# Kernel tuning notes

Measured on AMD Instinct MI355X. Metric: run time of the kernel, lower is better.

The kernel has to match this reference:

```python
import jax, jax.numpy as jnp
import numpy as np

BATCH, IN_DIM, GRID, OUT_DIM = 2048, 512, 32, 512


def setup_inputs() -> dict:
    key = jax.random.key(0)
    k_x, k_c = jax.random.split(key)
    x = jax.random.normal(k_x, (BATCH, IN_DIM), dtype=jnp.float32)
    fourier_coeffs = jax.random.normal(k_c, (2, IN_DIM, GRID, OUT_DIM), dtype=jnp.float32) / np.sqrt(GRID * OUT_DIM)
    bias = jnp.zeros((1, OUT_DIM), dtype=jnp.float32)
    return {"x": x, "fourier_coeffs": fourier_coeffs, "bias": bias}


def reference(x, fourier_coeffs, bias):
    # freqs: 1..GRID, shape (GRID,)
    freqs = jnp.arange(1, GRID + 1, dtype=x.dtype)
    kx = x[..., None] * freqs            # [B, I, G]
    cos_t = jnp.cos(kx)
    sin_t = jnp.sin(kx)
    # Equivalent to broadcast-multiply with coeffs then sum over grid and input dims:
    y = (jnp.einsum('big,igo->bo', cos_t, fourier_coeffs[0])
         + jnp.einsum('big,igo->bo', sin_t, fourier_coeffs[1]))
    return y + bias
```

## Files before the change

kernel.cpp:

```cpp
#include <hip/hip_runtime.h>
#include <hip/hip_bf16.h>
#include <stdint.h>

namespace {

constexpr int IDIM   = 512;
constexpr int ODIM   = 512;
constexpr int KTOT   = 32768;
constexpr int BM = 128, BN = 128, BK = 64;
constexpr int SPLITK = 8;
constexpr int KCHUNK = KTOT / SPLITK;
constexpr int NSTEP  = KCHUNK / BK;

typedef short    bf16x8 __attribute__((ext_vector_type(8)));
typedef float    f32x4  __attribute__((ext_vector_type(4)));
typedef float    f32x2  __attribute__((ext_vector_type(2)));
typedef uint32_t u32x4  __attribute__((ext_vector_type(4)));

__device__ __forceinline__ uint32_t f2bf1(float f) {
  union { float f; uint32_t u; } v; v.f = f;
  return (v.u + 0x7fffu + ((v.u >> 16) & 1u)) >> 16;
}
__device__ __forceinline__ uint32_t pk2(float lo, float hi) {
  return f2bf1(lo) | (f2bf1(hi) << 16);
}

__device__ __forceinline__ uint32_t pk2f(float lo, float hi) {
  union { float f; uint32_t u; } a, b; a.f = lo; b.f = hi;
  return __builtin_amdgcn_perm(b.u + 0x8000u, a.u + 0x8000u, 0x07060302u);
}

__device__ __forceinline__ void gload_lds16(const void* gsrc, const char* ldsdst) {
  __builtin_amdgcn_global_load_lds(
      (const __attribute__((address_space(1))) uint32_t*)(uintptr_t)gsrc,
      (__attribute__((address_space(3))) uint32_t*)(uint32_t)(uintptr_t)ldsdst,
      16, 0, 0);
}

#define WAIT_LGKM0   asm volatile("s_waitcnt lgkmcnt(0)" ::: "memory")
#define WAIT_VM(N)   asm volatile("s_waitcnt vmcnt(" #N ")" ::: "memory")
#define FENCE        asm volatile("" ::: "memory")

__global__ __launch_bounds__(256) void transpose_convert_kernel(const float* __restrict__ fc,
                                                                uint16_t* __restrict__ wt) {
  const int t = threadIdx.x, lane = t & 63, wave = t >> 6;
  const int bid = blockIdx.x;
  const int ot = bid & 3;
  const int kt = bid >> 2;
  const int o0 = ot * 128 + lane * 2;
  const int kb = kt * 128 + wave * 32;
  const float* src = fc + (size_t)kb * ODIM + o0;
  uint32_t w0[16], w1[16];
#pragma unroll
  for (int p = 0; p < 16; ++p) {
    f32x2 a = *(const f32x2*)(src + (size_t)(2 * p) * ODIM);
    f32x2 b = *(const f32x2*)(src + (size_t)(2 * p + 1) * ODIM);
    w0[p] = pk2(a.x, b.x);
    w1[p] = pk2(a.y, b.y);
  }
  uint16_t* dst0 = wt + (size_t)o0 * KTOT + kb;
  uint16_t* dst1 = dst0 + KTOT;
#pragma unroll
  for (int c = 0; c < 4; ++c) {
    *(u32x4*)(dst0 + c * 8) = *(const u32x4*)&w0[c * 4];
    *(u32x4*)(dst1 + c * 8) = *(const u32x4*)&w1[c * 4];
  }
}

__global__ __launch_bounds__(256) void init_bias_kernel(const float* __restrict__ bias,
                                                        float* __restrict__ out) {
  int i = blockIdx.x * 256 + threadIdx.x;
  ((f32x4*)out)[i] = ((const f32x4*)bias)[i & 127];
}

__global__ __launch_bounds__(256, 2) void fkan_gemm_kernel(const float* __restrict__ x,
                                                           const uint16_t* __restrict__ wt,
                                                           float* __restrict__ out) {
  __shared__ char lds[81920];

  const int t    = threadIdx.x;
  const int lane = t & 63;
  const int wave = t >> 6;

  int bid = blockIdx.x;
  int swz = (bid & 7) * 64 + (bid >> 3);
  const int bm = swz & 15;
  const int bn = (swz >> 4) & 3;
  const int bz = swz >> 6;

  const int row0  = bm * BM;
  const int col0  = bn * BN;
  const int kc0   = bz * KCHUNK;
  const int sflag = bz >> 2;
  const int ibase = (bz & 3) * 128;

  const int gr   = t & 127;
  const int ioff = t >> 7;
  const float* xp = x + (size_t)(row0 + gr) * IDIM + ibase + ioff;
  int awoff[4];
#pragma unroll
  for (int j = 0; j < 4; ++j)
    awoff[j] = gr * 128 + (((ioff * 4 + j) ^ (gr & 7)) << 4);

  const uint16_t* wptr[4];
  int wdst[4];
#pragma unroll
  for (int q = 0; q < 4; ++q) {
    int nl   = q * 32 + wave * 8 + (lane >> 3);
    int slot = lane & 7;
    wptr[q] = wt + (size_t)(col0 + nl) * KTOT + kc0 + ((slot ^ (nl & 7)) << 3);
    wdst[q] = q * 4096 + wave * 1024;
  }

  const int wm = wave >> 1, wn = wave & 1;
  int arow[4], ar7[4], bcol[4], bc7[4];
#pragma unroll
  for (int m = 0; m < 4; ++m) {
    int rr = wm * 64 + m * 16 + (lane & 15);
    arow[m] = rr * 128; ar7[m] = rr & 7;
    int cc = wn * 64 + m * 16 + (lane & 15);
    bcol[m] = cc * 128; bc7[m] = cc & 7;
  }

  f32x4 acc[4][4] = {};

  auto stageW = [&](int buf) {
#pragma unroll
    for (int q = 0; q < 4; ++q) {
      gload_lds16(wptr[q], lds + 32768 + buf * 16384 + wdst[q]);
      wptr[q] += BK;
    }
  };

  auto genA = [&](int abuf, float ang) {
    float s1, c1;
    __sincosf(ang, &s1, &c1);
    const float c2 = 2.f * c1 * c1 - 1.f;
    const float s2 = 2.f * s1 * c1;
    const float k2 = 2.f * c2;
    float po  = sflag ? s1   : c1;
    float pe  = sflag ? s2   : c2;
    float pom = sflag ? -s1  : c1;
    float pem = sflag ? 0.f  : 1.f;
    char* ab = lds + abuf * 16384;
#pragma unroll
    for (int grp = 0; grp < 4; ++grp) {
      u32x4 w;
#pragma unroll
      for (int u = 0; u < 4; ++u) {
        w[u] = pk2f(po, pe);
        float no = k2 * po - pom; pom = po; po = no;
        float ne = k2 * pe - pem; pem = pe; pe = ne;
      }
      *(u32x4*)(ab + awoff[grp]) = w;
    }
  };

  auto compute = [&](int wbuf, int abuf) {
    const char* ab = lds + abuf * 16384;
    const char* wb = lds + 32768 + wbuf * 16384;
#pragma unroll
    for (int ks = 0; ks < 2; ++ks) {
      const int ksb = ks * 4 + (lane >> 4);
      bf16x8 af[4], bfr[4];
#pragma unroll
      for (int m = 0; m < 4; ++m)
        af[m] = *(const bf16x8*)(ab + arow[m] + ((ksb ^ ar7[m]) << 4));
#pragma unroll
      for (int n = 0; n < 4; ++n)
        bfr[n] = *(const bf16x8*)(wb + bcol[n] + ((ksb ^ bc7[n]) << 4));
#pragma unroll
      for (int m = 0; m < 4; ++m)
#pragma unroll
        for (int n = 0; n < 4; ++n)
          acc[m][n] = __builtin_amdgcn_mfma_f32_16x16x32_bf16(af[m], bfr[n], acc[m][n], 0, 0, 0);
    }
  };

  float angCur  = xp[0];
  float angNext = xp[2];
  stageW(0);
  stageW(1);
  genA(0, angCur);
  WAIT_VM(4);
  WAIT_LGKM0;
  __builtin_amdgcn_s_barrier();
  FENCE;

  int wb_c = 0;
  int ws_c = 2;
  for (int st = 0; st < NSTEP; ++st) {
    const int ab = st & 1;
    if (st + 2 < NSTEP) {
      stageW(ws_c);
      ws_c = (ws_c == 2) ? 0 : ws_c + 1;
    }
    if (st + 1 < NSTEP) {
      float a = angNext;
      if (st + 2 < NSTEP) angNext = xp[2 * (st + 2)];
      genA(ab ^ 1, a);
    }
    compute(wb_c, ab);
    wb_c = (wb_c == 2) ? 0 : wb_c + 1;
    if (st + 1 < NSTEP) {
      WAIT_LGKM0;
      if (st + 2 < NSTEP) { WAIT_VM(4); } else { WAIT_VM(0); }
      __builtin_amdgcn_s_barrier();
      FENCE;
    }
  }

#pragma unroll
  for (int m = 0; m < 4; ++m) {
#pragma unroll
    for (int n = 0; n < 4; ++n) {
      int rr = row0 + wm * 64 + m * 16 + ((lane >> 4) << 2);
      int cc = col0 + wn * 64 + n * 16 + (lane & 15);
#pragma unroll
      for (int j = 0; j < 4; ++j)
        atomicAdd(out + (size_t)(rr + j) * ODIM + cc, acc[m][n][j]);
    }
  }
}

}

extern "C" void kernel_launch(void* const* d_in, const int* in_sizes, int n_in,
                              void* d_out, int out_size, void* d_ws, size_t ws_size,
                              hipStream_t stream) {
  const float* x    = (const float*)d_in[0];
  const float* fc   = (const float*)d_in[1];
  const float* bias = (const float*)d_in[2];
  float*    out = (float*)d_out;
  uint16_t* wt  = (uint16_t*)d_ws;

  transpose_convert_kernel<<<1024, 256, 0, stream>>>(fc, wt);
  init_bias_kernel<<<1024, 256, 0, stream>>>(bias, out);
  fkan_gemm_kernel<<<512, 256, 0, stream>>>(x, wt, out);
}
```

Before: 198.7 us.

## Fuse fp32-to-bf16 weight transpose into GEMM via register-staged loads

Removes the separate transpose/convert pre-pass that wrote a bf16 transposed copy of the coefficients to workspace. The GEMM now reads fp32 coefficients directly with per-lane strided loads into registers, converts them to bf16, and writes them to LDS in the swizzled layout. The weight pipeline goes from a triple-buffered async global-to-LDS scheme to double buffering through registers. This saves one full pass over the 64MB coefficient tensor, but the GEMM now reads twice the bytes per weight, holds 32 extra registers per thread, and exposes load latency behind a full vmcnt(0) wait each step.

```diff
diff --git a/kernel.cpp b/kernel.cpp
--- a/kernel.cpp
+++ b/kernel.cpp
@@ -14,58 +14,16 @@
 
 typedef short    bf16x8 __attribute__((ext_vector_type(8)));
 typedef float    f32x4  __attribute__((ext_vector_type(4)));
-typedef float    f32x2  __attribute__((ext_vector_type(2)));
 typedef uint32_t u32x4  __attribute__((ext_vector_type(4)));
-
-__device__ __forceinline__ uint32_t f2bf1(float f) {
-  union { float f; uint32_t u; } v; v.f = f;
-  return (v.u + 0x7fffu + ((v.u >> 16) & 1u)) >> 16;
-}
-__device__ __forceinline__ uint32_t pk2(float lo, float hi) {
-  return f2bf1(lo) | (f2bf1(hi) << 16);
-}
 
 __device__ __forceinline__ uint32_t pk2f(float lo, float hi) {
   union { float f; uint32_t u; } a, b; a.f = lo; b.f = hi;
   return __builtin_amdgcn_perm(b.u + 0x8000u, a.u + 0x8000u, 0x07060302u);
 }
 
-__device__ __forceinline__ void gload_lds16(const void* gsrc, const char* ldsdst) {
-  __builtin_amdgcn_global_load_lds(
-      (const __attribute__((address_space(1))) uint32_t*)(uintptr_t)gsrc,
-      (__attribute__((address_space(3))) uint32_t*)(uint32_t)(uintptr_t)ldsdst,
-      16, 0, 0);
-}
-
 #define WAIT_LGKM0   asm volatile("s_waitcnt lgkmcnt(0)" ::: "memory")
-#define WAIT_VM(N)   asm volatile("s_waitcnt vmcnt(" #N ")" ::: "memory")
+#define WAIT_VM0     asm volatile("s_waitcnt vmcnt(0)" ::: "memory")
 #define FENCE        asm volatile("" ::: "memory")
-
-__global__ __launch_bounds__(256) void transpose_convert_kernel(const float* __restrict__ fc,
-                                                                uint16_t* __restrict__ wt) {
-  const int t = threadIdx.x, lane = t & 63, wave = t >> 6;
-  const int bid = blockIdx.x;
-  const int ot = bid & 3;
-  const int kt = bid >> 2;
-  const int o0 = ot * 128 + lane * 2;
-  const int kb = kt * 128 + wave * 32;
-  const float* src = fc + (size_t)kb * ODIM + o0;
-  uint32_t w0[16], w1[16];
-#pragma unroll
-  for (int p = 0; p < 16; ++p) {
-    f32x2 a = *(const f32x2*)(src + (size_t)(2 * p) * ODIM);
-    f32x2 b = *(const f32x2*)(src + (size_t)(2 * p + 1) * ODIM);
-    w0[p] = pk2(a.x, b.x);
-    w1[p] = pk2(a.y, b.y);
-  }
-  uint16_t* dst0 = wt + (size_t)o0 * KTOT + kb;
-  uint16_t* dst1 = dst0 + KTOT;
-#pragma unroll
-  for (int c = 0; c < 4; ++c) {
-    *(u32x4*)(dst0 + c * 8) = *(const u32x4*)&w0[c * 4];
-    *(u32x4*)(dst1 + c * 8) = *(const u32x4*)&w1[c * 4];
-  }
-}
 
 __global__ __launch_bounds__(256) void init_bias_kernel(const float* __restrict__ bias,
                                                         float* __restrict__ out) {
@@ -74,9 +32,9 @@
 }
 
 __global__ __launch_bounds__(256, 2) void fkan_gemm_kernel(const float* __restrict__ x,
-                                                           const uint16_t* __restrict__ wt,
+                                                           const float* __restrict__ fc,
                                                            float* __restrict__ out) {
-  __shared__ char lds[81920];
+  __shared__ char lds[65536];
 
   const int t    = threadIdx.x;
   const int lane = t & 63;
@@ -102,14 +60,15 @@
   for (int j = 0; j < 4; ++j)
     awoff[j] = gr * 128 + (((ioff * 4 + j) ^ (gr & 7)) << 4);
 
-  const uint16_t* wptr[4];
-  int wdst[4];
+  int wko[4], wo[4], wldso[4];
 #pragma unroll
   for (int q = 0; q < 4; ++q) {
-    int nl   = q * 32 + wave * 8 + (lane >> 3);
-    int slot = lane & 7;
-    wptr[q] = wt + (size_t)(col0 + nl) * KTOT + kc0 + ((slot ^ (nl & 7)) << 3);
-    wdst[q] = q * 4096 + wave * 1024;
+    int idx = wave * 4 + q;
+    wko[q] = idx >> 1;
+    wo[q]  = (idx & 1) * 64 + lane;
+    int o = wo[q];
+    wldso[q] = (o >> 5) * 4096 + ((o >> 3) & 3) * 1024 +
+               (((o & 7) * 8 + (wko[q] ^ (o & 7))) << 4);
   }
 
   const int wm = wave >> 1, wn = wave & 1;
@@ -123,12 +82,27 @@
   }
 
   f32x4 acc[4][4] = {};
-
-  auto stageW = [&](int buf) {
+  float r[4][8];
+
+  auto stageLoad = [&](int st) {
+    const float* base = fc + (size_t)(kc0 + st * BK) * ODIM + col0;
 #pragma unroll
     for (int q = 0; q < 4; ++q) {
-      gload_lds16(wptr[q], lds + 32768 + buf * 16384 + wdst[q]);
-      wptr[q] += BK;
+      const float* s = base + (size_t)(wko[q] * 8) * ODIM + wo[q];
+#pragma unroll
+      for (int j = 0; j < 8; ++j)
+        r[q][j] = s[(size_t)j * ODIM];
+    }
+  };
+
+  auto stageWrite = [&](int buf) {
+#pragma unroll
+    for (int q = 0; q < 4; ++q) {
+      u32x4 w;
+#pragma unroll
+      for (int u = 0; u < 4; ++u)
+        w[u] = pk2f(r[q][2 * u], r[q][2 * u + 1]);
+      *(u32x4*)(lds + 32768 + buf * 16384 + wldso[q]) = w;
     }
   };
 
@@ -156,9 +130,9 @@
     }
   };
 
-  auto compute = [&](int wbuf, int abuf) {
-    const char* ab = lds + abuf * 16384;
-    const char* wb = lds + 32768 + wbuf * 16384;
+  auto compute = [&](int par) {
+    const char* ab = lds + par * 16384;
+    const char* wb = lds + 32768 + par * 16384;
 #pragma unroll
     for (int ks = 0; ks < 2; ++ks) {
       const int ksb = ks * 4 + (lane >> 4);
@@ -179,35 +153,32 @@
 
   float angCur  = xp[0];
   float angNext = xp[2];
-  stageW(0);
-  stageW(1);
+  stageLoad(0);
   genA(0, angCur);
-  WAIT_VM(4);
+  WAIT_VM0;
+  stageWrite(0);
   WAIT_LGKM0;
   __builtin_amdgcn_s_barrier();
   FENCE;
 
-  int wb_c = 0;
-  int ws_c = 2;
+  int par = 0;
   for (int st = 0; st < NSTEP; ++st) {
-    const int ab = st & 1;
-    if (st + 2 < NSTEP) {
-      stageW(ws_c);
-      ws_c = (ws_c == 2) ? 0 : ws_c + 1;
-    }
     if (st + 1 < NSTEP) {
+      stageLoad(st + 1);
       float a = angNext;
-      if (st + 2 < NSTEP) angNext = xp[2 * (st + 2)];
-      genA(ab ^ 1, a);
-    }
-    compute(wb_c, ab);
-    wb_c = (wb_c == 2) ? 0 : wb_c + 1;
+      int pf = (st + 2 < NSTEP) ? (st + 2) : (NSTEP - 1);
+      angNext = xp[2 * pf];
+      genA(par ^ 1, a);
+    }
+    compute(par);
     if (st + 1 < NSTEP) {
+      WAIT_VM0;
+      stageWrite(par ^ 1);
       WAIT_LGKM0;
-      if (st + 2 < NSTEP) { WAIT_VM(4); } else { WAIT_VM(0); }
       __builtin_amdgcn_s_barrier();
       FENCE;
     }
+    par ^= 1;
   }
 
 #pragma unroll
@@ -232,9 +203,8 @@
   const float* fc   = (const float*)d_in[1];
   const float* bias = (const float*)d_in[2];
   float*    out = (float*)d_out;
-  uint16_t* wt  = (uint16_t*)d_ws;
-
-  transpose_convert_kernel<<<1024, 256, 0, stream>>>(fc, wt);
+  (void)d_ws; (void)ws_size;
+
   init_bias_kernel<<<1024, 256, 0, stream>>>(bias, out);
-  fkan_gemm_kernel<<<512, 256, 0, stream>>>(x, wt, out);
-}
+  fkan_gemm_kernel<<<512, 256, 0, stream>>>(x, fc, out);
+}
```

Result: slower. 212.0 us (+6.7%).

## Generate Fourier A fragments in registers instead of staging through LDS

Applied to the files above, without the earlier changes.

Each wave now builds its own bf16 cos/sin MFMA A-fragments in registers. It loads x values directly and uses a sincos plus Chebyshev recurrence per fragment, instead of writing a shared A tile to LDS and reading it back. This removes the A-tile LDS stores and reads and shrinks shared memory from 80KB to 48KB. The main loop becomes a two-step unrolled loop with double-buffered x registers and a single vmcnt wait. The cost is extra VALU work: more sincos calls, and the trig generation is duplicated across the two waves that share rows. The vmcnt(8) wait also forces the newest weight stage to finish earlier than strictly needed.

```diff
diff --git a/kernel.cpp b/kernel.cpp
--- a/kernel.cpp
+++ b/kernel.cpp
@@ -24,7 +24,6 @@
 __device__ __forceinline__ uint32_t pk2(float lo, float hi) {
   return f2bf1(lo) | (f2bf1(hi) << 16);
 }
-
 __device__ __forceinline__ uint32_t pk2f(float lo, float hi) {
   union { float f; uint32_t u; } a, b; a.f = lo; b.f = hi;
   return __builtin_amdgcn_perm(b.u + 0x8000u, a.u + 0x8000u, 0x07060302u);
@@ -37,7 +36,6 @@
       16, 0, 0);
 }
 
-#define WAIT_LGKM0   asm volatile("s_waitcnt lgkmcnt(0)" ::: "memory")
 #define WAIT_VM(N)   asm volatile("s_waitcnt vmcnt(" #N ")" ::: "memory")
 #define FENCE        asm volatile("" ::: "memory")
 
@@ -76,11 +74,13 @@
 __global__ __launch_bounds__(256, 2) void fkan_gemm_kernel(const float* __restrict__ x,
                                                            const uint16_t* __restrict__ wt,
                                                            float* __restrict__ out) {
-  __shared__ char lds[81920];
+  __shared__ char lds[49152];
 
   const int t    = threadIdx.x;
   const int lane = t & 63;
   const int wave = t >> 6;
+  const int lid  = lane & 15;
+  const int hb   = lane >> 4;
 
   int bid = blockIdx.x;
   int swz = (bid & 7) * 64 + (bid >> 3);
@@ -94,14 +94,6 @@
   const int sflag = bz >> 2;
   const int ibase = (bz & 3) * 128;
 
-  const int gr   = t & 127;
-  const int ioff = t >> 7;
-  const float* xp = x + (size_t)(row0 + gr) * IDIM + ibase + ioff;
-  int awoff[4];
-#pragma unroll
-  for (int j = 0; j < 4; ++j)
-    awoff[j] = gr * 128 + (((ioff * 4 + j) ^ (gr & 7)) << 4);
-
   const uint16_t* wptr[4];
   int wdst[4];
 #pragma unroll
@@ -113,59 +105,69 @@
   }
 
   const int wm = wave >> 1, wn = wave & 1;
-  int arow[4], ar7[4], bcol[4], bc7[4];
-#pragma unroll
-  for (int m = 0; m < 4; ++m) {
-    int rr = wm * 64 + m * 16 + (lane & 15);
-    arow[m] = rr * 128; ar7[m] = rr & 7;
-    int cc = wn * 64 + m * 16 + (lane & 15);
-    bcol[m] = cc * 128; bc7[m] = cc & 7;
-  }
-
-  f32x4 acc[4][4] = {};
+  int bcol[4], bc7[4];
+#pragma unroll
+  for (int n = 0; n < 4; ++n) {
+    int cc = wn * 64 + n * 16 + lid;
+    bcol[n] = cc * 128; bc7[n] = cc & 7;
+  }
+
+  const float* xb0 = x + (size_t)(row0 + wm * 64 + lid) * IDIM + ibase;
+  const float n0f = (float)(hb * 8 + 1);
+
+  f32x4  acc[4][4] = {};
+  bf16x8 af[2][4];
 
   auto stageW = [&](int buf) {
 #pragma unroll
     for (int q = 0; q < 4; ++q) {
-      gload_lds16(wptr[q], lds + 32768 + buf * 16384 + wdst[q]);
+      gload_lds16(wptr[q], lds + buf * 16384 + wdst[q]);
       wptr[q] += BK;
     }
   };
 
-  auto genA = [&](int abuf, float ang) {
-    float s1, c1;
-    __sincosf(ang, &s1, &c1);
-    const float c2 = 2.f * c1 * c1 - 1.f;
-    const float s2 = 2.f * s1 * c1;
-    const float k2 = 2.f * c2;
-    float po  = sflag ? s1   : c1;
-    float pe  = sflag ? s2   : c2;
-    float pom = sflag ? -s1  : c1;
-    float pem = sflag ? 0.f  : 1.f;
-    char* ab = lds + abuf * 16384;
-#pragma unroll
-    for (int grp = 0; grp < 4; ++grp) {
-      u32x4 w;
-#pragma unroll
-      for (int u = 0; u < 4; ++u) {
-        w[u] = pk2f(po, pe);
-        float no = k2 * po - pom; pom = po; po = no;
-        float ne = k2 * pe - pem; pem = pe; pe = ne;
+  auto loadX = [&](float (&dst)[4][2], int st) {
+#pragma unroll
+    for (int m = 0; m < 4; ++m) {
+      const float* p = xb0 + (size_t)(m * 16) * IDIM + st * 2;
+      dst[m][0] = p[0]; dst[m][1] = p[1];
+    }
+  };
+
+  auto genAll = [&](const float (&xc)[4][2]) {
+#pragma unroll
+    for (int m = 0; m < 4; ++m) {
+#pragma unroll
+      for (int ks = 0; ks < 2; ++ks) {
+        float xx = xc[m][ks];
+        float s1, c1; __sincosf(xx, &s1, &c1);
+        float sn, cn; __sincosf(n0f * xx, &sn, &cn);
+        const float k2 = 2.f * c1;
+        float cur, prev;
+        if (sflag == 0) { cur = cn; prev = fmaf(cn, c1,  sn * s1); }
+        else            { cur = sn; prev = fmaf(sn, c1, -cn * s1); }
+        float v[8];
+        v[0] = cur;
+#pragma unroll
+        for (int j = 1; j < 8; ++j) {
+          float nx = fmaf(k2, cur, -prev);
+          prev = cur; cur = nx; v[j] = nx;
+        }
+        union { u32x4 u4; bf16x8 b8; } cvt;
+#pragma unroll
+        for (int u = 0; u < 4; ++u)
+          cvt.u4[u] = pk2f(v[2 * u], v[2 * u + 1]);
+        af[ks][m] = cvt.b8;
       }
-      *(u32x4*)(ab + awoff[grp]) = w;
-    }
-  };
-
-  auto compute = [&](int wbuf, int abuf) {
-    const char* ab = lds + abuf * 16384;
-    const char* wb = lds + 32768 + wbuf * 16384;
+    }
+  };
+
+  auto compute = [&](int wbuf) {
+    const char* wb = lds + wbuf * 16384;
 #pragma unroll
     for (int ks = 0; ks < 2; ++ks) {
-      const int ksb = ks * 4 + (lane >> 4);
-      bf16x8 af[4], bfr[4];
-#pragma unroll
-      for (int m = 0; m < 4; ++m)
-        af[m] = *(const bf16x8*)(ab + arow[m] + ((ksb ^ ar7[m]) << 4));
+      const int ksb = ks * 4 + hb;
+      bf16x8 bfr[4];
 #pragma unroll
       for (int n = 0; n < 4; ++n)
         bfr[n] = *(const bf16x8*)(wb + bcol[n] + ((ksb ^ bc7[n]) << 4));
@@ -173,41 +175,35 @@
       for (int m = 0; m < 4; ++m)
 #pragma unroll
         for (int n = 0; n < 4; ++n)
-          acc[m][n] = __builtin_amdgcn_mfma_f32_16x16x32_bf16(af[m], bfr[n], acc[m][n], 0, 0, 0);
-    }
-  };
-
-  float angCur  = xp[0];
-  float angNext = xp[2];
+          acc[m][n] = __builtin_amdgcn_mfma_f32_16x16x32_bf16(af[ks][m], bfr[n], acc[m][n], 0, 0, 0);
+    }
+  };
+
+  float xA[4][2], xB[4][2];
+
+  loadX(xA, 0);
   stageW(0);
   stageW(1);
-  genA(0, angCur);
   WAIT_VM(4);
-  WAIT_LGKM0;
   __builtin_amdgcn_s_barrier();
   FENCE;
 
-  int wb_c = 0;
-  int ws_c = 2;
-  for (int st = 0; st < NSTEP; ++st) {
-    const int ab = st & 1;
-    if (st + 2 < NSTEP) {
-      stageW(ws_c);
-      ws_c = (ws_c == 2) ? 0 : ws_c + 1;
-    }
+  auto iter = [&](int st, const float (&xcur)[4][2], float (&xnxt)[4][2]) {
+    if (st + 2 < NSTEP) stageW((st + 2) % 3);
+    if (st + 1 < NSTEP) loadX(xnxt, st + 1);
+    genAll(xcur);
+    compute(st % 3);
     if (st + 1 < NSTEP) {
-      float a = angNext;
-      if (st + 2 < NSTEP) angNext = xp[2 * (st + 2)];
-      genA(ab ^ 1, a);
-    }
-    compute(wb_c, ab);
-    wb_c = (wb_c == 2) ? 0 : wb_c + 1;
-    if (st + 1 < NSTEP) {
-      WAIT_LGKM0;
-      if (st + 2 < NSTEP) { WAIT_VM(4); } else { WAIT_VM(0); }
+      WAIT_VM(8);
       __builtin_amdgcn_s_barrier();
       FENCE;
     }
+  };
+
+#pragma unroll 1
+  for (int st2 = 0; st2 < NSTEP; st2 += 2) {
+    iter(st2,     xA, xB);
+    iter(st2 + 1, xB, xA);
   }
 
 #pragma unroll
@@ -215,7 +211,7 @@
 #pragma unroll
     for (int n = 0; n < 4; ++n) {
       int rr = row0 + wm * 64 + m * 16 + ((lane >> 4) << 2);
-      int cc = col0 + wn * 64 + n * 16 + (lane & 15);
+      int cc = col0 + wn * 64 + n * 16 + lid;
 #pragma unroll
       for (int j = 0; j < 4; ++j)
         atomicAdd(out + (size_t)(rr + j) * ODIM + cc, acc[m][n][j]);
```

After: 248.2 us. 1.25x slower.

## Load B fragments directly from global into registers, drop LDS staging

Applied to the files above, without the earlier changes.

Weight tiles are no longer staged through LDS with global_load_lds and a triple buffer. Each wave now loads its MFMA B fragments straight from global memory into double-buffered registers, one step ahead. This shrinks LDS from 80KB to 32KB and removes the LDS reads for B, but each weight element is now loaded twice, once per wave row (wm). It also adds register pressure and waits on vmcnt(0) every step, which reduces how much loads overlap with compute.

```diff
diff --git a/kernel.cpp b/kernel.cpp
--- a/kernel.cpp
+++ b/kernel.cpp
@@ -24,21 +24,13 @@
 __device__ __forceinline__ uint32_t pk2(float lo, float hi) {
   return f2bf1(lo) | (f2bf1(hi) << 16);
 }
-
 __device__ __forceinline__ uint32_t pk2f(float lo, float hi) {
   union { float f; uint32_t u; } a, b; a.f = lo; b.f = hi;
   return __builtin_amdgcn_perm(b.u + 0x8000u, a.u + 0x8000u, 0x07060302u);
 }
 
-__device__ __forceinline__ void gload_lds16(const void* gsrc, const char* ldsdst) {
-  __builtin_amdgcn_global_load_lds(
-      (const __attribute__((address_space(1))) uint32_t*)(uintptr_t)gsrc,
-      (__attribute__((address_space(3))) uint32_t*)(uint32_t)(uintptr_t)ldsdst,
-      16, 0, 0);
-}
-
 #define WAIT_LGKM0   asm volatile("s_waitcnt lgkmcnt(0)" ::: "memory")
-#define WAIT_VM(N)   asm volatile("s_waitcnt vmcnt(" #N ")" ::: "memory")
+#define WAIT_VM0     asm volatile("s_waitcnt vmcnt(0)" ::: "memory")
 #define FENCE        asm volatile("" ::: "memory")
 
 __global__ __launch_bounds__(256) void transpose_convert_kernel(const float* __restrict__ fc,
@@ -76,11 +68,13 @@
 __global__ __launch_bounds__(256, 2) void fkan_gemm_kernel(const float* __restrict__ x,
                                                            const uint16_t* __restrict__ wt,
                                                            float* __restrict__ out) {
-  __shared__ char lds[81920];
+  __shared__ char lds[32768];
 
   const int t    = threadIdx.x;
   const int lane = t & 63;
   const int wave = t >> 6;
+  const int lid  = lane & 15;
+  const int hb   = lane >> 4;
 
   int bid = blockIdx.x;
   int swz = (bid & 7) * 64 + (bid >> 3);
@@ -102,34 +96,27 @@
   for (int j = 0; j < 4; ++j)
     awoff[j] = gr * 128 + (((ioff * 4 + j) ^ (gr & 7)) << 4);
 
-  const uint16_t* wptr[4];
-  int wdst[4];
-#pragma unroll
-  for (int q = 0; q < 4; ++q) {
-    int nl   = q * 32 + wave * 8 + (lane >> 3);
-    int slot = lane & 7;
-    wptr[q] = wt + (size_t)(col0 + nl) * KTOT + kc0 + ((slot ^ (nl & 7)) << 3);
-    wdst[q] = q * 4096 + wave * 1024;
-  }
-
   const int wm = wave >> 1, wn = wave & 1;
-  int arow[4], ar7[4], bcol[4], bc7[4];
+  int arow[4], ar7[4];
 #pragma unroll
   for (int m = 0; m < 4; ++m) {
-    int rr = wm * 64 + m * 16 + (lane & 15);
+    int rr = wm * 64 + m * 16 + lid;
     arow[m] = rr * 128; ar7[m] = rr & 7;
-    int cc = wn * 64 + m * 16 + (lane & 15);
-    bcol[m] = cc * 128; bc7[m] = cc & 7;
-  }
+  }
+
+  const uint16_t* bp[4];
+#pragma unroll
+  for (int n = 0; n < 4; ++n)
+    bp[n] = wt + (size_t)(col0 + wn * 64 + n * 16 + lid) * KTOT + kc0 + hb * 8;
 
   f32x4 acc[4][4] = {};
 
-  auto stageW = [&](int buf) {
-#pragma unroll
-    for (int q = 0; q < 4; ++q) {
-      gload_lds16(wptr[q], lds + 32768 + buf * 16384 + wdst[q]);
-      wptr[q] += BK;
-    }
+  auto loadB = [&](bf16x8 (&d)[8], int st) {
+#pragma unroll
+    for (int ks = 0; ks < 2; ++ks)
+#pragma unroll
+      for (int n = 0; n < 4; ++n)
+        d[ks * 4 + n] = *(const bf16x8*)(bp[n] + st * BK + ks * 32);
   };
 
   auto genA = [&](int abuf, float ang) {
@@ -156,58 +143,56 @@
     }
   };
 
-  auto compute = [&](int wbuf, int abuf) {
-    const char* ab = lds + abuf * 16384;
-    const char* wb = lds + 32768 + wbuf * 16384;
+  auto compute = [&](int par, const bf16x8 (&bfr)[8]) {
+    const char* ab = lds + par * 16384;
 #pragma unroll
     for (int ks = 0; ks < 2; ++ks) {
-      const int ksb = ks * 4 + (lane >> 4);
-      bf16x8 af[4], bfr[4];
+      const int ksb = ks * 4 + hb;
+      bf16x8 af[4];
 #pragma unroll
       for (int m = 0; m < 4; ++m)
         af[m] = *(const bf16x8*)(ab + arow[m] + ((ksb ^ ar7[m]) << 4));
 #pragma unroll
-      for (int n = 0; n < 4; ++n)
-        bfr[n] = *(const bf16x8*)(wb + bcol[n] + ((ksb ^ bc7[n]) << 4));
-#pragma unroll
       for (int m = 0; m < 4; ++m)
 #pragma unroll
         for (int n = 0; n < 4; ++n)
-          acc[m][n] = __builtin_amdgcn_mfma_f32_16x16x32_bf16(af[m], bfr[n], acc[m][n], 0, 0, 0);
-    }
-  };
+          acc[m][n] = __builtin_amdgcn_mfma_f32_16x16x32_bf16(af[m], bfr[ks * 4 + n], acc[m][n], 0, 0, 0);
+    }
+  };
+
+  bf16x8 bA[8], bB[8];
 
   float angCur  = xp[0];
   float angNext = xp[2];
-  stageW(0);
-  stageW(1);
+  loadB(bA, 0);
   genA(0, angCur);
-  WAIT_VM(4);
+  WAIT_VM0;
   WAIT_LGKM0;
   __builtin_amdgcn_s_barrier();
   FENCE;
 
-  int wb_c = 0;
-  int ws_c = 2;
-  for (int st = 0; st < NSTEP; ++st) {
-    const int ab = st & 1;
-    if (st + 2 < NSTEP) {
-      stageW(ws_c);
-      ws_c = (ws_c == 2) ? 0 : ws_c + 1;
-    }
+  int par = 0;
+  auto iter = [&](int st, const bf16x8 (&bC)[8], bf16x8 (&bN)[8]) {
     if (st + 1 < NSTEP) {
+      loadB(bN, st + 1);
       float a = angNext;
       if (st + 2 < NSTEP) angNext = xp[2 * (st + 2)];
-      genA(ab ^ 1, a);
-    }
-    compute(wb_c, ab);
-    wb_c = (wb_c == 2) ? 0 : wb_c + 1;
+      genA(par ^ 1, a);
+    }
+    compute(par, bC);
     if (st + 1 < NSTEP) {
+      WAIT_VM0;
       WAIT_LGKM0;
-      if (st + 2 < NSTEP) { WAIT_VM(4); } else { WAIT_VM(0); }
       __builtin_amdgcn_s_barrier();
       FENCE;
     }
+    par ^= 1;
+  };
+
+#pragma unroll 1
+  for (int st2 = 0; st2 < NSTEP; st2 += 2) {
+    iter(st2,     bA, bB);
+    iter(st2 + 1, bB, bA);
   }
 
 #pragma unroll
@@ -215,7 +200,7 @@
 #pragma unroll
     for (int n = 0; n < 4; ++n) {
       int rr = row0 + wm * 64 + m * 16 + ((lane >> 4) << 2);
-      int cc = col0 + wn * 64 + n * 16 + (lane & 15);
+      int cc = col0 + wn * 64 + n * 16 + lid;
 #pragma unroll
       for (int j = 0; j < 4; ++j)
         atomicAdd(out + (size_t)(rr + j) * ODIM + cc, acc[m][n][j]);
```

After: 266.1 us. +33.9%, slower.
